# Performance work log

Measured on AMD Instinct MI355X. Metric: run time of the kernel, lower is better.

## Reference

```python
import jax, jax.numpy as jnp
import numpy as np

N_NODES = 30000
N_EDGES = 480000
IN_SIZE = 256
EDGE_FEAT = 32
N_TOWERS = 4
DELTA = 2.5


def setup_inputs():
    key = jax.random.key(0)
    ks = jax.random.split(key, 8)
    T, d = N_TOWERS, IN_SIZE // N_TOWERS
    m_in = 2 * d + EDGE_FEAT                 # M: Linear(2*tower_in+edge_feat -> tower_in)
    u_in = (4 * 3 + 1) * d                   # U: Linear((n_agg*n_scaler+1)*tower_in -> tower_out)
    return {
        "n_feat": jax.random.normal(ks[0], (N_NODES, IN_SIZE), jnp.float32),
        "e_feat": jax.random.normal(ks[1], (N_EDGES, EDGE_FEAT), jnp.float32),
        "src": jax.random.randint(ks[2], (N_EDGES,), 0, N_NODES),
        "dst": jax.random.randint(ks[3], (N_EDGES,), 0, N_NODES),
        "M_w": jax.random.normal(ks[4], (T, d, m_in), jnp.float32) * (1.0 / np.sqrt(m_in)),
        "M_b": jnp.zeros((T, d), jnp.float32),
        "U_w": jax.random.normal(ks[5], (T, d, u_in), jnp.float32) * (1.0 / np.sqrt(u_in)),
        "U_b": jnp.zeros((T, d), jnp.float32),
        "bn_gamma": jnp.ones((T, d), jnp.float32),
        "bn_beta": jnp.zeros((T, d), jnp.float32),
        "mix_w": jax.random.normal(ks[6], (IN_SIZE, IN_SIZE), jnp.float32) * (1.0 / np.sqrt(IN_SIZE)),
        "mix_b": jnp.zeros((IN_SIZE,), jnp.float32),
    }


def reference(n_feat, e_feat, src, dst, M_w, M_b, U_w, U_b, bn_gamma, bn_beta, mix_w, mix_b):
    N, F = n_feat.shape
    T, d, _ = M_w.shape
    E = src.shape[0]
    h = n_feat.reshape(N, T, d)                                   # towers split the feature dim
    ef = jnp.broadcast_to(e_feat[:, None, :], (E, T, e_feat.shape[1]))
    f = jnp.concatenate([h[src], h[dst], ef], axis=-1)            # [E,T,2d+ef]
    msg = jnp.einsum('eti,toi->eto', f, M_w) + M_b                # per-edge message, [E,T,d]

    deg = jax.ops.segment_sum(jnp.ones((E,), msg.dtype), dst, num_segments=N)  # in-degree
    degc = jnp.maximum(deg, 1.0)[:, None, None]
    s = jax.ops.segment_sum(msg, dst, num_segments=N)
    ssq = jax.ops.segment_sum(msg * msg, dst, num_segments=N)
    mean = s / degc
    var = jax.nn.relu(ssq / degc - mean * mean)                   # DGL aggregate_var
    std = jnp.sqrt(var + 1e-30)                                   # DGL aggregate_std
    has = (deg > 0.0)[:, None, None]
    mx = jnp.where(has, jax.ops.segment_max(msg, dst, num_segments=N), 0.0)
    mn = jnp.where(has, jax.ops.segment_min(msg, dst, num_segments=N), 0.0)
    agg = jnp.concatenate([mean, mx, mn, std], axis=-1)           # [N,T,4d]

    logd = jnp.log(deg + 1.0)
    amp = (logd / DELTA)[:, None, None]                            # amplification scaler
    att = jnp.where(deg > 0.0, DELTA / jnp.maximum(logd, 1e-12), 0.0)[:, None, None]  # attenuation
    hsc = jnp.concatenate([agg, agg * amp, agg * att], axis=-1)   # [N,T,12d]

    u_in = jnp.concatenate([h, hsc], axis=-1)                     # [N,T,13d]
    u = jnp.einsum('nti,toi->nto', u_in, U_w) + U_b               # [N,T,d]
    mu = jnp.mean(u, axis=0)
    v = jnp.mean((u - mu) ** 2, axis=0)
    u = (u - mu) / jnp.sqrt(v + 1e-5) * bn_gamma + bn_beta        # BatchNorm1d (training mode)

    h_cat = u.reshape(N, F)
    mixed = h_cat @ mix_w.T + mix_b
    mixed = jnp.where(mixed > 0, mixed, 0.01 * mixed)             # LeakyReLU mixing layer
    out = mixed + n_feat                                          # residual (in_size==out_size)
    return jax.nn.relu(out)                                       # last == 0 -> ReLU
```

## Files before the change

### kernel.cpp

```cpp
#include <hip/hip_runtime.h>
#include <math.h>

constexpr float DELTA_ = 2.5f;
#define BN_BLOCKS 512
#define NPB 8

typedef __attribute__((ext_vector_type(8))) short bf16x8;
typedef __attribute__((ext_vector_type(8))) _Float16 f16x8;
typedef __attribute__((ext_vector_type(4))) float f32x4;

__device__ inline ushort bf16h(float x){
  union { float f; unsigned u; } v; v.f = x;
  unsigned r = v.u + 0x7fffu + ((v.u >> 16) & 1u);
  return (ushort)(r >> 16);
}
__device__ inline float bf16f(ushort h){
  union { unsigned u; float f; } v; v.u = ((unsigned)h) << 16;
  return v.f;
}

__global__ __launch_bounds__(256) void k_tU(const float* __restrict__ Uw, ushort* __restrict__ Wpk2){
  int i = blockIdx.x*256 + threadIdx.x;
  if (i >= 4*192*320) return;
  int k   = i % 320;
  int col = (i/320) % 192;
  int t   = i/(320*192);
  int path = col >> 6, o = col & 63;
  float v = 0.f;
  int src = -1;
  if (k < 64){ if (path == 0) src = k; }
  else        src = k + path*256;
  if (src >= 0) v = Uw[((size_t)(t*64 + o))*832 + src];
  Wpk2[i] = bf16h(v);
}

__global__ __launch_bounds__(256) void k_tMm(const float* __restrict__ mixw, ushort* __restrict__ Wm2){
  int i = blockIdx.x*256 + threadIdx.x;
  if (i >= 256*256) return;
  Wm2[i] = bf16h(mixw[i]);
}

__global__ __launch_bounds__(256) void k_tW(const float* __restrict__ Mw, _Float16* __restrict__ Wall){
  int i = blockIdx.x*256 + threadIdx.x;
  if (i >= 4*4*3*64*8) return;
  int j     = i & 7;
  int lane  = (i >> 3) & 63;
  int slice = (i / 512) % 3;
  int cb    = (i / 1536) % 4;
  int t     = i / 6144;
  int ch = t*64 + cb*16 + (lane & 15);
  int k  = slice*32 + ((lane >> 4) & 3)*8 + j;
  int off = (k < 64) ? k : (128 + (k - 64));
  Wall[i] = (_Float16)Mw[(size_t)ch*160 + off];
}

__global__ __launch_bounds__(256) void k_xh(const float* __restrict__ nf, ushort* __restrict__ X2, int N){
  for (long i = blockIdx.x*256 + threadIdx.x; i < (long)N*256; i += (long)gridDim.x*256){
    int n = (int)(i >> 8), c = (int)(i & 255);
    int t = c >> 6, d = c & 63;
    int j = d >> 3, pos = d & 7;
    float v = nf[i];
    ushort hi = bf16h(v);
    size_t base = (((size_t)n*4 + t)*40 + j)*16;
    X2[base + pos]     = hi;
    X2[base + 8 + pos] = bf16h(v - bf16f(hi));
  }
}

__global__ __launch_bounds__(256) void k_hist(const int* __restrict__ dstv, int* __restrict__ cnt, int E){
  int e = blockIdx.x*256 + threadIdx.x;
  if (e < E) atomicAdd(&cnt[dstv[e]], 1);
}

__global__ __launch_bounds__(256) void k_scan1(const int* __restrict__ cnt, int* __restrict__ offs,
                                               int* __restrict__ bsum, int N){
  __shared__ int lds[256];
  int i = threadIdx.x;
  int g = blockIdx.x*256 + i;
  int v = (g < N) ? cnt[g] : 0;
  int acc = v;
  lds[i] = acc; __syncthreads();
  for (int s = 1; s < 256; s <<= 1){
    int t = (i >= s) ? lds[i - s] : 0;
    __syncthreads();
    acc += t; lds[i] = acc;
    __syncthreads();
  }
  if (g < N) offs[g] = acc - v;
  if (i == 255) bsum[blockIdx.x] = acc;
}

__global__ __launch_bounds__(256) void k_scan2(int* __restrict__ bsum, int NB){
  __shared__ int lds[256];
  int i = threadIdx.x;
  int v = (i < NB) ? bsum[i] : 0;
  int acc = v;
  lds[i] = acc; __syncthreads();
  for (int s = 1; s < 256; s <<= 1){
    int t = (i >= s) ? lds[i - s] : 0;
    __syncthreads();
    acc += t; lds[i] = acc;
    __syncthreads();
  }
  if (i < NB) bsum[i] = acc - v;
}

__global__ __launch_bounds__(256) void k_scan3(int* __restrict__ offs, const int* __restrict__ bsum, int N, int E){
  int g = blockIdx.x*256 + threadIdx.x;
  if (g < N) offs[g] += bsum[blockIdx.x];
  if (g == 0) offs[N] = E;
}

__global__ __launch_bounds__(256) void k_fill(const int* __restrict__ dstv, const int* __restrict__ offs,
                                              int* __restrict__ cur, int* __restrict__ elist, int E){
  int e = blockIdx.x*256 + threadIdx.x;
  if (e < E){
    int d = dstv[e];
    elist[offs[d] + atomicAdd(&cur[d], 1)] = e;
  }
}

__global__ __launch_bounds__(256) void k_perm(const int* __restrict__ elist, const int* __restrict__ srcv,
                                              const float* __restrict__ efeat,
                                              int* __restrict__ esrc, _Float16* __restrict__ efh, int E){
  int g = blockIdx.x*256 + threadIdx.x;
  int pos = g >> 3;
  int q   = g & 7;
  if (pos >= E) return;
  int e = elist[pos];
  if (q == 0) esrc[pos] = srcv[e];
  float4 v = *(const float4*)(efeat + (size_t)e*32 + q*4);
  union { ushort4 u; _Float16 h[4]; } cv;
  cv.h[0] = (_Float16)v.x; cv.h[1] = (_Float16)v.y;
  cv.h[2] = (_Float16)v.z; cv.h[3] = (_Float16)v.w;
  *(ushort4*)(efh + (size_t)pos*32 + q*4) = cv.u;
}

__global__ __launch_bounds__(256) void k_ab(const float* __restrict__ nf, const float* __restrict__ Mw,
                                            const float* __restrict__ Mb,
                                            _Float16* __restrict__ nfh, float* __restrict__ B, int N){
  int c = threadIdx.x;
  int t = __builtin_amdgcn_readfirstlane(threadIdx.x >> 6);
  float wd[64];
  const float* row = Mw + (size_t)c*160 + 64;
#pragma unroll
  for (int k = 0; k < 64; k += 4){
    float4 b = *(const float4*)(row + k);
    wd[k]=b.x; wd[k+1]=b.y; wd[k+2]=b.z; wd[k+3]=b.w;
  }
  float bias = Mb[c];
  for (int n = blockIdx.x; n < N; n += gridDim.x){
    const float* h = nf + (size_t)n*256 + t*64;
    float sb = 0.f;
#pragma unroll
    for (int k = 0; k < 64; k += 4){
      float4 h4 = *(const float4*)(h + k);
      sb = fmaf(wd[k], h4.x, sb);
      sb = fmaf(wd[k+1], h4.y, sb);
      sb = fmaf(wd[k+2], h4.z, sb);
      sb = fmaf(wd[k+3], h4.w, sb);
    }
    B[(size_t)n*256 + c] = sb + bias;
    nfh[(size_t)n*256 + c] = (_Float16)nf[(size_t)n*256 + c];
  }
}

__global__ __launch_bounds__(256) void k_agg(const int* __restrict__ offs, const int* __restrict__ esrc,
                                             const _Float16* __restrict__ efh,
                                             const _Float16* __restrict__ nfh, const float* __restrict__ B,
                                             const _Float16* __restrict__ Wall,
                                             ushort* __restrict__ X2, float* __restrict__ sc, int N, int E){
  __shared__ _Float16 eps[256][68];
  int tid = threadIdx.x;
  int lane = tid & 63, wv = tid >> 6;
  int li = lane & 15, kq = lane >> 4;
  int c = tid;
  int tw = c >> 6, d = c & 63;

  int n0 = blockIdx.x * NPB;
  if (n0 >= N) return;
  int n1 = n0 + NPB; if (n1 > N) n1 = N;
  int oS = offs[n0], oE = offs[n1];

  f16x8 bf[4][3];
#pragma unroll
  for (int cb = 0; cb < 4; ++cb)
#pragma unroll
    for (int sl = 0; sl < 3; ++sl)
      bf[cb][sl] = *(const f16x8*)(Wall + ((((size_t)wv*4 + cb)*3 + sl)*64 + lane)*8);

  int cur = n0;
  int curstart = oS;
  int nextoff = offs[n0 + 1];
  float s = 0.f, ss = 0.f;
  float mx = -__builtin_huge_valf(), mn = __builtin_huge_valf();

#define FINALIZE(CNT)                                                             \
  {                                                                                \
    float b = B[(size_t)cur*256 + c];                                              \
    float deg = (float)(CNT);                                                      \
    float degc = fmaxf(deg, 1.f);                                                  \
    float inv = 1.f / degc;                                                        \
    float S  = fmaf(deg, b, s);                                                    \
    float SS = fmaf(deg, b*b, fmaf(2.f*b, s, ss));                                 \
    float mean = S * inv;                                                          \
    float var  = fmaxf(SS * inv - mean*mean, 0.f);                                 \
    float sd   = sqrtf(var + 1e-30f);                                              \
    float MX = ((CNT) > 0) ? (b + mx) : 0.f;                                       \
    float MN = ((CNT) > 0) ? (b + mn) : 0.f;                                       \
    size_t xb = (((size_t)cur*4 + tw)*40)*16;                                      \
    { int kk = 64 + d;       ushort h2 = bf16h(mean);                              \
      X2[xb + (kk>>3)*16 + (kk&7)] = h2;                                           \
      X2[xb + (kk>>3)*16 + 8 + (kk&7)] = bf16h(mean - bf16f(h2)); }                \
    { int kk = 128 + d;      ushort h2 = bf16h(MX);                                \
      X2[xb + (kk>>3)*16 + (kk&7)] = h2;                                           \
      X2[xb + (kk>>3)*16 + 8 + (kk&7)] = bf16h(MX - bf16f(h2)); }                  \
    { int kk = 192 + d;      ushort h2 = bf16h(MN);                                \
      X2[xb + (kk>>3)*16 + (kk&7)] = h2;                                           \
      X2[xb + (kk>>3)*16 + 8 + (kk&7)] = bf16h(MN - bf16f(h2)); }                  \
    { int kk = 256 + d;      ushort h2 = bf16h(sd);                                \
      X2[xb + (kk>>3)*16 + (kk&7)] = h2;                                           \
      X2[xb + (kk>>3)*16 + 8 + (kk&7)] = bf16h(sd - bf16f(h2)); }                  \
    if (tid == 0){                                                                 \
      float logd = logf(deg + 1.f);                                                \
      sc[(size_t)cur*2]     = logd * (1.f / DELTA_);                               \
      sc[(size_t)cur*2 + 1] = ((CNT) > 0) ? (DELTA_ / fmaxf(logd, 1e-12f)) : 0.f;  \
    }                                                                              \
  }

  for (int w0 = oS; w0 < oE; w0 += 64){
    __syncthreads();
#pragma unroll
    for (int ch4 = 0; ch4 < 4; ++ch4){
      int pos = w0 + ch4*16 + li; if (pos > E - 1) pos = E - 1;
      int src = esrc[pos];
      const _Float16* hp = nfh + (size_t)src*256 + wv*64;
      f16x8 a0 = *(const f16x8*)(hp + kq*8);
      f16x8 a1 = *(const f16x8*)(hp + 32 + kq*8);
      f16x8 a2 = *(const f16x8*)(efh + (size_t)pos*32 + kq*8);
#pragma unroll
      for (int cb = 0; cb < 4; ++cb){
        f32x4 acc = __builtin_amdgcn_mfma_f32_16x16x32_f16(a0, bf[cb][0], (f32x4)0.f, 0, 0, 0);
        acc = __builtin_amdgcn_mfma_f32_16x16x32_f16(a1, bf[cb][1], acc, 0, 0, 0);
        acc = __builtin_amdgcn_mfma_f32_16x16x32_f16(a2, bf[cb][2], acc, 0, 0, 0);
        union { ushort4 u4; _Float16 h[4]; } st;
        st.h[0] = (_Float16)acc[0];
        st.h[1] = (_Float16)acc[1];
        st.h[2] = (_Float16)acc[2];
        st.h[3] = (_Float16)acc[3];
        *(ushort4*)(&eps[wv*64 + cb*16 + li][ch4*16 + kq*4]) = st.u4;
      }
    }
    __syncthreads();

    int wend = w0 + 64; if (wend > oE) wend = oE;
    for (int g = 0; g < 64; g += 4){
      if (w0 + g >= wend) break;
      union { ushort4 u4; _Float16 h[4]; } ld;
      ld.u4 = *(const ushort4*)(&eps[c][g]);
#pragma unroll
      for (int r = 0; r < 4; ++r){
        int idx = w0 + g + r;
        if (idx >= wend) break;
        while (idx == nextoff){
          FINALIZE(nextoff - curstart)
          curstart = nextoff;
          ++cur;
          nextoff = offs[cur + 1];
          s = 0.f; ss = 0.f;
          mx = -__builtin_huge_valf(); mn = __builtin_huge_valf();
        }
        float m = (float)ld.h[r];
        s += m;
        ss = fmaf(m, m, ss);
        mx = fmaxf(mx, m);
        mn = fminf(mn, m);
      }
    }
  }

  while (cur < n1){
    FINALIZE(nextoff - curstart)
    curstart = nextoff;
    ++cur;
    if (cur < n1) nextoff = offs[cur + 1];
    s = 0.f; ss = 0.f;
    mx = -__builtin_huge_valf(); mn = __builtin_huge_valf();
  }
#undef FINALIZE
}

__global__ __launch_bounds__(256) void k_u(const ushort* __restrict__ X2, const ushort* __restrict__ Wpk2,
                                           const float* __restrict__ sc, const float* __restrict__ Ub,
                                           float* __restrict__ uout, int Nn){
  __shared__ float su[64][68];
  int tid = threadIdx.x;
  int t   = blockIdx.y;
  int nbase = blockIdx.x*64;
  int lane = tid & 63, wv = tid >> 6;
  int li = lane & 15, kc = lane >> 4;
  int cbase = wv*48;

  f32x4 acc[4][3];
#pragma unroll
  for (int ri = 0; ri < 4; ++ri)
#pragma unroll
    for (int ci = 0; ci < 3; ++ci) acc[ri][ci] = (f32x4)0.f;

  const ushort* wb = Wpk2 + (size_t)t*192*320;

#pragma unroll 2
  for (int kt = 0; kt < 10; ++kt){
    bf16x8 ah[4], al[4], bh[3];
#pragma unroll
    for (int ri = 0; ri < 4; ++ri){
      int row = nbase + ri*16 + li;
      if (row >= Nn) row = Nn - 1;
      const ushort* ap = X2 + (((size_t)row*4 + t)*40 + kt*4 + kc)*16;
      ah[ri] = *(const bf16x8*)(ap);
      al[ri] = *(const bf16x8*)(ap + 8);
    }
#pragma unroll
    for (int ci = 0; ci < 3; ++ci){
      int col = cbase + ci*16 + li;
      bh[ci] = *(const bf16x8*)(wb + (size_t)col*320 + kt*32 + kc*8);
    }
#pragma unroll
    for (int ci = 0; ci < 3; ++ci)
#pragma unroll
      for (int ri = 0; ri < 4; ++ri){
        acc[ri][ci] = __builtin_amdgcn_mfma_f32_16x16x32_bf16(ah[ri], bh[ci], acc[ri][ci], 0, 0, 0);
        acc[ri][ci] = __builtin_amdgcn_mfma_f32_16x16x32_bf16(al[ri], bh[ci], acc[ri][ci], 0, 0, 0);
      }
  }

#define Y1_STORE(CI, OB) { _Pragma("unroll") for (int ri = 0; ri < 4; ++ri)               \
    { _Pragma("unroll") for (int r = 0; r < 4; ++r)                                        \
      su[ri*16 + kc*4 + r][(OB) + li] = acc[ri][CI][r]; } }
#define Y_ADD(CI, OB, SCOFF) { _Pragma("unroll") for (int ri = 0; ri < 4; ++ri)           \
    { _Pragma("unroll") for (int r = 0; r < 4; ++r){                                       \
      int node = ri*16 + kc*4 + r;                                                        \
      int gn = nbase + node; int gnc = (gn < Nn) ? gn : (Nn - 1);                          \
      float scl = sc[(size_t)gnc*2 + (SCOFF)];                                            \
      su[node][(OB) + li] += scl * acc[ri][CI][r]; } } }

  if (wv == 0){ Y1_STORE(0, 0)  Y1_STORE(1, 16) Y1_STORE(2, 32) }
  else if (wv == 1){ Y1_STORE(0, 48) }
  __syncthreads();
  if (wv == 1){ Y_ADD(1, 0, 0)  Y_ADD(2, 16, 0) }
  else if (wv == 2){ Y_ADD(0, 32, 0) Y_ADD(1, 48, 0) }
  __syncthreads();
  if (wv == 2){ Y_ADD(2, 0, 1) }
  else if (wv == 3){ Y_ADD(0, 16, 1) Y_ADD(1, 32, 1) Y_ADD(2, 48, 1) }
  __syncthreads();
#undef Y1_STORE
#undef Y_ADD

  for (int idx = tid; idx < 64*16; idx += 256){
    int n = idx >> 4, o4 = (idx & 15)*4;
    int gn = nbase + n;
    if (gn < Nn){
      float4 v = *(float4*)(&su[n][o4]);
      const float* ubp = Ub + t*64 + o4;
      v.x += ubp[0]; v.y += ubp[1]; v.z += ubp[2]; v.w += ubp[3];
      *(float4*)(&uout[(size_t)gn*256 + t*64 + o4]) = v;
    }
  }
}

__global__ __launch_bounds__(256) void k_bnstat(const float* __restrict__ u, float* __restrict__ part, int N){
  int c = threadIdx.x;
  int b = blockIdx.x;
  float s = 0.f, ss = 0.f;
  for (int n = b; n < N; n += gridDim.x){
    float v = u[(size_t)n*256 + c];
    s += v;
    ss = fmaf(v, v, ss);
  }
  part[(size_t)b*512 + c]       = s;
  part[(size_t)b*512 + 256 + c] = ss;
}

__global__ __launch_bounds__(256) void k_bnfin(const float* __restrict__ part, const float* __restrict__ gam,
                                               const float* __restrict__ bet, float* __restrict__ bnsc, int N){
  int c = threadIdx.x;
  float s = 0.f, ss = 0.f;
  for (int b = 0; b < BN_BLOCKS; ++b){
    s  += part[(size_t)b*512 + c];
    ss += part[(size_t)b*512 + 256 + c];
  }
  float invN = 1.f / (float)N;
  float mu  = s * invN;
  float ex2 = ss * invN;
  float var = fmaxf(ex2 - mu*mu, 0.f);
  float inv = 1.f / sqrtf(var + 1e-5f);
  float scale = gam[c] * inv;
  bnsc[c]       = scale;
  bnsc[256 + c] = bet[c] - mu*scale;
}

__global__ __launch_bounds__(256) void k_xm(const float* __restrict__ u, const float* __restrict__ bnsc,
                                            ushort* __restrict__ X2m, int N){
  for (long i = blockIdx.x*256 + threadIdx.x; i < (long)N*256; i += (long)gridDim.x*256){
    int n = (int)(i >> 8), c = (int)(i & 255);
    float v = fmaf(u[i], bnsc[c], bnsc[256 + c]);
    int j = c >> 3, pos = c & 7;
    size_t base = ((size_t)n*32 + j)*16;
    ushort hi = bf16h(v);
    X2m[base + pos]     = hi;
    X2m[base + 8 + pos] = bf16h(v - bf16f(hi));
  }
}

__global__ __launch_bounds__(256) void k_mix(const ushort* __restrict__ X2m, const ushort* __restrict__ Wm2,
                                             const float* __restrict__ mixb, const float* __restrict__ nf,
                                             float* __restrict__ outp, int Nn){
  int tid = threadIdx.x;
  int nbase = blockIdx.x*64;
  int lane = tid & 63, wv = tid >> 6;
  int li = lane & 15, kc = lane >> 4;

  f32x4 acc[4][4];
#pragma unroll
  for (int ri = 0; ri < 4; ++ri)
#pragma unroll
    for (int ci = 0; ci < 4; ++ci) acc[ri][ci] = (f32x4)0.f;

#pragma unroll 2
  for (int kt = 0; kt < 8; ++kt){
    bf16x8 ah[4], al[4], bh[4];
#pragma unroll
    for (int ri = 0; ri < 4; ++ri){
      int row = nbase + ri*16 + li;
      if (row >= Nn) row = Nn - 1;
      const ushort* ap = X2m + (((size_t)row*32 + kt*4 + kc))*16;
      ah[ri] = *(const bf16x8*)(ap);
      al[ri] = *(const bf16x8*)(ap + 8);
    }
#pragma unroll
    for (int ci = 0; ci < 4; ++ci){
      int col = wv*64 + ci*16 + li;
      bh[ci] = *(const bf16x8*)(Wm2 + (size_t)col*256 + kt*32 + kc*8);
    }
#pragma unroll
    for (int ci = 0; ci < 4; ++ci)
#pragma unroll
      for (int ri = 0; ri < 4; ++ri){
        acc[ri][ci] = __builtin_amdgcn_mfma_f32_16x16x32_bf16(ah[ri], bh[ci], acc[ri][ci], 0, 0, 0);
        acc[ri][ci] = __builtin_amdgcn_mfma_f32_16x16x32_bf16(al[ri], bh[ci], acc[ri][ci], 0, 0, 0);
      }
  }

#pragma unroll
  for (int ri = 0; ri < 4; ++ri){
#pragma unroll
    for (int r = 0; r < 4; ++r){
      int node = ri*16 + kc*4 + r;
      int gn = nbase + node;
      if (gn < Nn){
#pragma unroll
        for (int ci = 0; ci < 4; ++ci){
          int col = wv*64 + ci*16 + li;
          float m = acc[ri][ci][r] + mixb[col];
          m = (m > 0.f) ? m : 0.01f*m;
          float o = m + nf[(size_t)gn*256 + col];
          outp[(size_t)gn*256 + col] = fmaxf(o, 0.f);
        }
      }
    }
  }
}

extern "C" void kernel_launch(void* const* d_in, const int* in_sizes, int n_in,
                              void* d_out, int out_size, void* d_ws, size_t ws_size,
                              hipStream_t stream){
  const float* nf   = (const float*)d_in[0];
  const float* ef   = (const float*)d_in[1];
  const int*   srcv = (const int*)  d_in[2];
  const int*   dstv = (const int*)  d_in[3];
  const float* Mw   = (const float*)d_in[4];
  const float* Mb   = (const float*)d_in[5];
  const float* Uw   = (const float*)d_in[6];
  const float* Ub   = (const float*)d_in[7];
  const float* gam  = (const float*)d_in[8];
  const float* bet  = (const float*)d_in[9];
  const float* mixw = (const float*)d_in[10];
  const float* mixb = (const float*)d_in[11];
  int N = in_sizes[0] / 256;
  int E = in_sizes[2];
  float* out = (float*)d_out;

  char* wp = (char*)d_ws;
  auto alloc = [&](size_t bytes){
    char* p = wp;
    wp += (bytes + 1023) & ~(size_t)1023;
    return (void*)p;
  };
  int*      cnt   = (int*)     alloc((size_t)N*4);
  int*      offs  = (int*)     alloc((size_t)(N+1)*4);
  int*      cur   = (int*)     alloc((size_t)N*4);
  int*      bsum  = (int*)     alloc(256*4);
  int*      elist = (int*)     alloc((size_t)E*4);
  int*      esrc  = (int*)     alloc((size_t)E*4);
  size_t ealias   = (size_t)E*32*2;
  size_t malias   = (size_t)N*512*2;
  char*     shbuf = (char*)    alloc(ealias > malias ? ealias : malias);
  _Float16* efh   = (_Float16*)shbuf;
  ushort*   X2m   = (ushort*)  shbuf;
  _Float16* nfh   = (_Float16*)alloc((size_t)N*256*2);
  float*    B     = (float*)   alloc((size_t)N*256*4);
  float*    sc    = (float*)   alloc((size_t)N*2*4);
  float*    part  = (float*)   alloc((size_t)BN_BLOCKS*512*4);
  float*    bnsc  = (float*)   alloc(512*4);
  ushort*   X2    = (ushort*)  alloc((size_t)N*4*40*16*2);
  ushort*   Wpk2  = (ushort*)  alloc((size_t)4*192*320*2);
  ushort*   Wm2   = (ushort*)  alloc((size_t)256*256*2);
  _Float16* Wall  = (_Float16*)alloc((size_t)4*4*3*64*8*2);

  hipMemsetAsync(cnt,  0, (size_t)N*4,  stream);
  hipMemsetAsync(cur,  0, (size_t)N*4,  stream);

  k_tU  <<<(4*192*320 + 255)/256, 256, 0, stream>>>(Uw, Wpk2);
  k_tMm <<<(256*256 + 255)/256, 256, 0, stream>>>(mixw, Wm2);
  k_tW  <<<(4*4*3*64*8 + 255)/256, 256, 0, stream>>>(Mw, Wall);
  k_hist<<<(E + 255)/256, 256, 0, stream>>>(dstv, cnt, E);
  k_ab  <<<2048, 256, 0, stream>>>(nf, Mw, Mb, nfh, B, N);
  k_xh  <<<2048, 256, 0, stream>>>(nf, X2, N);

  int NB = (N + 255)/256;
  k_scan1<<<NB, 256, 0, stream>>>(cnt, offs, bsum, N);
  k_scan2<<<1, 256, 0, stream>>>(bsum, NB);
  k_scan3<<<NB, 256, 0, stream>>>(offs, bsum, N, E);
  k_fill <<<(E + 255)/256, 256, 0, stream>>>(dstv, offs, cur, elist, E);
  k_perm <<<(E*8 + 255)/256, 256, 0, stream>>>(elist, srcv, ef, esrc, efh, E);

  k_agg<<<(N + NPB - 1)/NPB, 256, 0, stream>>>(offs, esrc, efh, nfh, B, Wall, X2, sc, N, E);

  dim3 ugrid((N + 63)/64, 4);
  k_u<<<ugrid, 256, 0, stream>>>(X2, Wpk2, sc, Ub, out, N);

  k_bnstat<<<BN_BLOCKS, 256, 0, stream>>>(out, part, N);
  k_bnfin <<<1, 256, 0, stream>>>(part, gam, bet, bnsc, N);
  k_xm   <<<2048, 256, 0, stream>>>(out, bnsc, X2m, N);
  k_mix  <<<(N + 63)/64, 256, 0, stream>>>(X2m, Wm2, mixb, nf, out, N);
}
```

Baseline: 453.6 us.

## Fold bf16 split conversions into producer and consumer kernels

The hi/lo bf16 split of node features, formerly a separate pass, is now written by k_ab, which already reads every feature. The BatchNorm apply plus bf16 split, formerly done by k_xm, now happens on the fly in the mixing GEMM, which reads raw fp32 u and the BN scale/shift directly. This removes two full-size intermediate passes and the aliased X2m buffer. The cost is that every wave in a mixing block redoes the conversion for the shared A rows, and the GEMM now reads and writes `out` in place, with a barrier before the epilogue stores.

```diff
diff --git a/kernel.cpp b/kernel.cpp
--- a/kernel.cpp
+++ b/kernel.cpp
@@ -52,19 +52,6 @@
   int k  = slice*32 + ((lane >> 4) & 3)*8 + j;
   int off = (k < 64) ? k : (128 + (k - 64));
   Wall[i] = (_Float16)Mw[(size_t)ch*160 + off];
-}
-
-__global__ __launch_bounds__(256) void k_xh(const float* __restrict__ nf, ushort* __restrict__ X2, int N){
-  for (long i = blockIdx.x*256 + threadIdx.x; i < (long)N*256; i += (long)gridDim.x*256){
-    int n = (int)(i >> 8), c = (int)(i & 255);
-    int t = c >> 6, d = c & 63;
-    int j = d >> 3, pos = d & 7;
-    float v = nf[i];
-    ushort hi = bf16h(v);
-    size_t base = (((size_t)n*4 + t)*40 + j)*16;
-    X2[base + pos]     = hi;
-    X2[base + 8 + pos] = bf16h(v - bf16f(hi));
-  }
 }
 
 __global__ __launch_bounds__(256) void k_hist(const int* __restrict__ dstv, int* __restrict__ cnt, int E){
@@ -138,9 +125,12 @@
 
 __global__ __launch_bounds__(256) void k_ab(const float* __restrict__ nf, const float* __restrict__ Mw,
                                             const float* __restrict__ Mb,
-                                            _Float16* __restrict__ nfh, float* __restrict__ B, int N){
+                                            _Float16* __restrict__ nfh, float* __restrict__ B,
+                                            ushort* __restrict__ X2, int N){
   int c = threadIdx.x;
   int t = __builtin_amdgcn_readfirstlane(threadIdx.x >> 6);
+  int d = c & 63;
+  int jj = d >> 3, pp = d & 7;
   float wd[64];
   const float* row = Mw + (size_t)c*160 + 64;
 #pragma unroll
@@ -161,7 +151,12 @@
       sb = fmaf(wd[k+3], h4.w, sb);
     }
     B[(size_t)n*256 + c] = sb + bias;
-    nfh[(size_t)n*256 + c] = (_Float16)nf[(size_t)n*256 + c];
+    float v = nf[(size_t)n*256 + c];
+    nfh[(size_t)n*256 + c] = (_Float16)v;
+    ushort hi = bf16h(v);
+    size_t base = (((size_t)n*4 + t)*40 + jj)*16;
+    X2[base + pp]     = hi;
+    X2[base + 8 + pp] = bf16h(v - bf16f(hi));
   }
 }
 
@@ -399,20 +394,8 @@
   bnsc[256 + c] = bet[c] - mu*scale;
 }
 
-__global__ __launch_bounds__(256) void k_xm(const float* __restrict__ u, const float* __restrict__ bnsc,
-                                            ushort* __restrict__ X2m, int N){
-  for (long i = blockIdx.x*256 + threadIdx.x; i < (long)N*256; i += (long)gridDim.x*256){
-    int n = (int)(i >> 8), c = (int)(i & 255);
-    float v = fmaf(u[i], bnsc[c], bnsc[256 + c]);
-    int j = c >> 3, pos = c & 7;
-    size_t base = ((size_t)n*32 + j)*16;
-    ushort hi = bf16h(v);
-    X2m[base + pos]     = hi;
-    X2m[base + 8 + pos] = bf16h(v - bf16f(hi));
-  }
-}
-
-__global__ __launch_bounds__(256) void k_mix(const ushort* __restrict__ X2m, const ushort* __restrict__ Wm2,
+__global__ __launch_bounds__(256) void k_mix(const float* __restrict__ u, const ushort* __restrict__ Wm2,
+                                             const float* __restrict__ bnsc,
                                              const float* __restrict__ mixb, const float* __restrict__ nf,
                                              float* __restrict__ outp, int Nn){
   int tid = threadIdx.x;
@@ -428,14 +411,33 @@
 
 #pragma unroll 2
   for (int kt = 0; kt < 8; ++kt){
+    int k0 = kt*32 + kc*8;
+    float4 s40 = *(const float4*)(bnsc + k0);
+    float4 s41 = *(const float4*)(bnsc + k0 + 4);
+    float4 h40 = *(const float4*)(bnsc + 256 + k0);
+    float4 h41 = *(const float4*)(bnsc + 256 + k0 + 4);
     bf16x8 ah[4], al[4], bh[4];
 #pragma unroll
     for (int ri = 0; ri < 4; ++ri){
       int row = nbase + ri*16 + li;
       if (row >= Nn) row = Nn - 1;
-      const ushort* ap = X2m + (((size_t)row*32 + kt*4 + kc))*16;
-      ah[ri] = *(const bf16x8*)(ap);
-      al[ri] = *(const bf16x8*)(ap + 8);
+      const float* up = u + (size_t)row*256 + k0;
+      float4 v0 = *(const float4*)(up);
+      float4 v1 = *(const float4*)(up + 4);
+      float x[8];
+      x[0] = fmaf(v0.x, s40.x, h40.x); x[1] = fmaf(v0.y, s40.y, h40.y);
+      x[2] = fmaf(v0.z, s40.z, h40.z); x[3] = fmaf(v0.w, s40.w, h40.w);
+      x[4] = fmaf(v1.x, s41.x, h41.x); x[5] = fmaf(v1.y, s41.y, h41.y);
+      x[6] = fmaf(v1.z, s41.z, h41.z); x[7] = fmaf(v1.w, s41.w, h41.w);
+      union { bf16x8 v; ushort u[8]; } hh, ll;
+#pragma unroll
+      for (int q = 0; q < 8; ++q){
+        ushort hb = bf16h(x[q]);
+        hh.u[q] = hb;
+        ll.u[q] = bf16h(x[q] - bf16f(hb));
+      }
+      ah[ri] = hh.v;
+      al[ri] = ll.v;
     }
 #pragma unroll
     for (int ci = 0; ci < 4; ++ci){
@@ -451,6 +453,7 @@
       }
   }
 
+  __syncthreads();
 #pragma unroll
   for (int ri = 0; ri < 4; ++ri){
 #pragma unroll
@@ -502,11 +505,7 @@
   int*      bsum  = (int*)     alloc(256*4);
   int*      elist = (int*)     alloc((size_t)E*4);
   int*      esrc  = (int*)     alloc((size_t)E*4);
-  size_t ealias   = (size_t)E*32*2;
-  size_t malias   = (size_t)N*512*2;
-  char*     shbuf = (char*)    alloc(ealias > malias ? ealias : malias);
-  _Float16* efh   = (_Float16*)shbuf;
-  ushort*   X2m   = (ushort*)  shbuf;
+  _Float16* efh   = (_Float16*)alloc((size_t)E*32*2);
   _Float16* nfh   = (_Float16*)alloc((size_t)N*256*2);
   float*    B     = (float*)   alloc((size_t)N*256*4);
   float*    sc    = (float*)   alloc((size_t)N*2*4);
@@ -524,8 +523,7 @@
   k_tMm <<<(256*256 + 255)/256, 256, 0, stream>>>(mixw, Wm2);
   k_tW  <<<(4*4*3*64*8 + 255)/256, 256, 0, stream>>>(Mw, Wall);
   k_hist<<<(E + 255)/256, 256, 0, stream>>>(dstv, cnt, E);
-  k_ab  <<<2048, 256, 0, stream>>>(nf, Mw, Mb, nfh, B, N);
-  k_xh  <<<2048, 256, 0, stream>>>(nf, X2, N);
+  k_ab  <<<2048, 256, 0, stream>>>(nf, Mw, Mb, nfh, B, X2, N);
 
   int NB = (N + 255)/256;
   k_scan1<<<NB, 256, 0, stream>>>(cnt, offs, bsum, N);
@@ -541,6 +539,5 @@
 
   k_bnstat<<<BN_BLOCKS, 256, 0, stream>>>(out, part, N);
   k_bnfin <<<1, 256, 0, stream>>>(part, gam, bet, bnsc, N);
-  k_xm   <<<2048, 256, 0, stream>>>(out, bnsc, X2m, N);
-  k_mix  <<<(N + 63)/64, 256, 0, stream>>>(X2m, Wm2, mixb, nf, out, N);
-}
+  k_mix  <<<(N + 63)/64, 256, 0, stream>>>(out, Wm2, bnsc, mixb, nf, out, N);
+}
```

After: 450.3 us. Within noise of the previous version (-0.7%).
